# Kernel optimization log

Measured on AMD Instinct MI355X. Metric: run time of the kernel, lower is better.

The kernel has to match this reference:

```python
import jax, jax.numpy as jnp
import numpy as np

B, C, N = 4, 64, 100000   # batch, num_bev_features, points per batch
NY, NX = 496, 432         # BEV grid (nz == 1)
PILLAR = 0.16


def setup_inputs() -> dict:
    key = jax.random.key(0)
    k1, k2, k3, k4 = jax.random.split(key, 4)
    point_feature = jax.random.normal(k1, (B, C, N), dtype=jnp.float32)
    # lidar points: [total, 4] = (batch_idx, x, y, z); each batch has exactly N rows
    bidx = jnp.repeat(jnp.arange(B, dtype=jnp.float32), N)[:, None]
    x = jax.random.uniform(k2, (B * N, 1), minval=0.0, maxval=69.12)
    y = jax.random.uniform(k3, (B * N, 1), minval=-39.68, maxval=39.68)
    z = jax.random.uniform(k4, (B * N, 1), minval=-3.0, maxval=1.0)
    points = jnp.concatenate([bidx, x, y, z], axis=1)
    # voxel_coords only used for batch_size = max(col0)+1
    voxel_coords = jnp.concatenate(
        [bidx.astype(jnp.int32),
         jnp.zeros((B * N, 3), dtype=jnp.int32)], axis=1)
    return {"point_feature": point_feature, "points": points,
            "voxel_coords": voxel_coords}


def _scatter_one(feat, pts_b):
    # feat: [C, N], pts_b: [N, 4]
    x = pts_b[:, 1]
    y = pts_b[:, 2]
    x_idx = jnp.clip(jnp.floor((x - x.min()) / PILLAR), 0, NX - 1).astype(jnp.int32)
    y_idx = jnp.clip(jnp.floor((y - y.min()) / PILLAR), 0, NY - 1).astype(jnp.int32)
    grid = jnp.zeros((C, NY, NX), dtype=feat.dtype)
    return grid.at[:, y_idx, x_idx].set(feat)


def reference(point_feature, points, voxel_coords):
    batch_size = point_feature.shape[0]  # == voxel_coords[:,0].max()+1 by construction
    n = point_feature.shape[2]
    # points are laid out contiguously per batch (col0 == batch idx), so the
    # boolean mask `lidar[:,0]==b` is equivalent to this reshape.
    pts = points.reshape(batch_size, n, points.shape[1])
    spatial_features = jax.vmap(_scatter_one)(point_feature, pts)  # [B, C, NY, NX]
    return spatial_features
```

## Files before the change

kernel.cpp:

```cpp
#include <hip/hip_runtime.h>
#include <stdint.h>

#define BATCH 4
#define CH 64
#define NPT 100000
#define NY 496
#define NX 432
#define NYNX (NY * NX)
#define INV_PILLAR 6.25f

typedef float vfloat4 __attribute__((ext_vector_type(4)));

#define MINBITS_OFF 0
#define WINNER_OFF  256
#define WINNER_BYTES ((size_t)BATCH * NYNX * sizeof(int))
#define FEATT_OFF   ((WINNER_OFF + WINNER_BYTES + 255) & ~(size_t)255)
#define FEATT_BYTES ((size_t)BATCH * (NPT + 1) * CH * sizeof(unsigned short))
#define WS_NEEDED   (FEATT_OFF + FEATT_BYTES)

__device__ __forceinline__ unsigned int f2sortable(float f) {
    unsigned int u = __float_as_uint(f);
    return (u & 0x80000000u) ? ~u : (u | 0x80000000u);
}
__device__ __forceinline__ float sortable2f(unsigned int u) {
    unsigned int b = (u & 0x80000000u) ? (u ^ 0x80000000u) : ~u;
    return __uint_as_float(b);
}
__device__ __forceinline__ unsigned short f2bf(float f) {
    unsigned int u = __float_as_uint(f);
    unsigned int r = u + 0x7FFFu + ((u >> 16) & 1u);
    return (unsigned short)(r >> 16);
}

#define CHUNKS_PER_BATCH 64
#define PTS_PER_CHUNK ((NPT + CHUNKS_PER_BATCH - 1) / CHUNKS_PER_BATCH)

__global__ void minred_kernel(const float* __restrict__ points,
                              unsigned int* __restrict__ minbits) {
    int b = blockIdx.x / CHUNKS_PER_BATCH;
    int chunk = blockIdx.x % CHUNKS_PER_BATCH;
    int lo = chunk * PTS_PER_CHUNK;
    int hi = min(lo + PTS_PER_CHUNK, NPT);
    const vfloat4* pts = (const vfloat4*)points + (size_t)b * NPT;
    float mx = 3.0e38f, my = 3.0e38f;
    for (int i = lo + threadIdx.x; i < hi; i += blockDim.x) {
        vfloat4 p = pts[i];
        mx = fminf(mx, p.y);
        my = fminf(my, p.z);
    }
    #pragma unroll
    for (int off = 32; off; off >>= 1) {
        mx = fminf(mx, __shfl_xor(mx, off));
        my = fminf(my, __shfl_xor(my, off));
    }
    if ((threadIdx.x & 63) == 0) {
        atomicMin(&minbits[2 * b],     f2sortable(mx));
        atomicMin(&minbits[2 * b + 1], f2sortable(my));
    }
}

__global__ void winner_kernel(const float* __restrict__ points,
                              const unsigned int* __restrict__ minbits,
                              int* __restrict__ winner) {
    int i = blockIdx.x * blockDim.x + threadIdx.x;
    if (i >= BATCH * NPT) return;
    int b = i / NPT;
    int li = i - b * NPT;
    vfloat4 p = ((const vfloat4*)points)[i];
    float xmin = sortable2f(minbits[2 * b]);
    float ymin = sortable2f(minbits[2 * b + 1]);
    float fx = fminf(fmaxf(floorf((p.y - xmin) * INV_PILLAR), 0.0f), (float)(NX - 1));
    float fy = fminf(fmaxf(floorf((p.z - ymin) * INV_PILLAR), 0.0f), (float)(NY - 1));
    int xi = (int)fx;
    int yi = (int)fy;
    atomicMax(&winner[(b * NY + yi) * NX + xi], li + 1);
}

#define NTILES ((NPT + 1 + 63) / 64)
__global__ void transpose_kernel(const float* __restrict__ feat,
                                 unsigned short* __restrict__ feat_t) {
    __shared__ float tile[CH][65];
    int b = blockIdx.x / NTILES;
    int n0 = (blockIdx.x % NTILES) * 64;
    int t = threadIdx.x;

    int l16 = t & 15;
    int crow = t >> 4;
    int nt4 = l16 * 4;
    if (n0 + nt4 + 3 < NPT) {
        #pragma unroll
        for (int k = 0; k < 4; ++k) {
            int c = crow + 16 * k;
            vfloat4 v = __builtin_nontemporal_load(
                (const vfloat4*)(feat + ((size_t)b * CH + c) * NPT + n0 + nt4));
            tile[c][nt4 + 0] = v.x;
            tile[c][nt4 + 1] = v.y;
            tile[c][nt4 + 2] = v.z;
            tile[c][nt4 + 3] = v.w;
        }
    } else {
        #pragma unroll
        for (int k = 0; k < 4; ++k) {
            int c = crow + 16 * k;
            for (int j = 0; j < 4; ++j) {
                int n = n0 + nt4 + j;
                tile[c][nt4 + j] = (n < NPT) ? feat[((size_t)b * CH + c) * NPT + n] : 0.0f;
            }
        }
    }
    __syncthreads();

    int c8 = (t & 7) * 8;
    int nr = t >> 3;
    #pragma unroll
    for (int k = 0; k < 2; ++k) {
        int nit = nr + 32 * k;
        int n = n0 + nit;
        if (n < NPT) {
            unsigned int w0 = (unsigned int)f2bf(tile[c8 + 0][nit]) |
                              ((unsigned int)f2bf(tile[c8 + 1][nit]) << 16);
            unsigned int w1 = (unsigned int)f2bf(tile[c8 + 2][nit]) |
                              ((unsigned int)f2bf(tile[c8 + 3][nit]) << 16);
            unsigned int w2 = (unsigned int)f2bf(tile[c8 + 4][nit]) |
                              ((unsigned int)f2bf(tile[c8 + 5][nit]) << 16);
            unsigned int w3 = (unsigned int)f2bf(tile[c8 + 6][nit]) |
                              ((unsigned int)f2bf(tile[c8 + 7][nit]) << 16);
            *(uint4*)(feat_t + ((size_t)b * (NPT + 1) + n) * CH + c8) =
                make_uint4(w0, w1, w2, w3);
        } else if (n == NPT) {
            *(uint4*)(feat_t + ((size_t)b * (NPT + 1) + n) * CH + c8) =
                make_uint4(0u, 0u, 0u, 0u);
        }
    }
}

#define QUADS_PER_BATCH (NYNX / 4)
__global__ void scatter_kernel(const unsigned short* __restrict__ feat_t,
                               const int* __restrict__ winner,
                               float* __restrict__ out) {
    int s = blockIdx.x * blockDim.x + threadIdx.x;
    if (s >= BATCH * QUADS_PER_BATCH) return;
    int b = s / QUADS_PER_BATCH;
    int yx0 = (s - b * QUADS_PER_BATCH) * 4;
    int4 w4 = *(const int4*)(winner + (size_t)b * NYNX + yx0);
    const unsigned short* fb = feat_t + (size_t)b * (NPT + 1) * CH;
    int wv[4] = {w4.x, w4.y, w4.z, w4.w};
    const uint4* col[4];
    #pragma unroll
    for (int i = 0; i < 4; ++i) {
        int c = (wv[i] < 0) ? NPT : (wv[i] - 1);
        col[i] = (const uint4*)(fb + (size_t)c * CH);
    }
    float* ob = out + (size_t)b * CH * NYNX + yx0;
    #pragma unroll
    for (int g = 0; g < 4; ++g) {
        uint4 ua[4], ub[4];
        #pragma unroll
        for (int i = 0; i < 4; ++i) {
            ua[i] = col[i][2 * g];
            ub[i] = col[i][2 * g + 1];
        }
        #pragma unroll
        for (int c = 0; c < 16; ++c) {
            int pair = c >> 1;
            vfloat4 v;
            #pragma unroll
            for (int i = 0; i < 4; ++i) {
                unsigned int src = (pair < 4) ? (&ua[i].x)[pair] : (&ub[i].x)[pair - 4];
                v[i] = __uint_as_float((c & 1) ? (src & 0xFFFF0000u) : (src << 16));
            }
            __builtin_nontemporal_store(
                v, (vfloat4*)(ob + (size_t)(16 * g + c) * NYNX));
        }
    }
}

__global__ void scatter_fallback_kernel(const float* __restrict__ feat,
                                        const int* __restrict__ winner,
                                        float* __restrict__ out) {
    int cell = blockIdx.x * blockDim.x + threadIdx.x;
    if (cell >= BATCH * NYNX) return;
    int b = cell / NYNX;
    int yx = cell - b * NYNX;
    int w = winner[cell];
    int ws_ = (w > 0) ? (w - 1) : 0;
    const float* fb = feat + (size_t)b * CH * NPT;
    float* ob = out + (size_t)b * CH * NYNX + yx;
    #pragma unroll 16
    for (int c = 0; c < CH; ++c) {
        float v = fb[(size_t)c * NPT + ws_];
        ob[(size_t)c * NYNX] = (w > 0) ? v : 0.0f;
    }
}

extern "C" void kernel_launch(void* const* d_in, const int* in_sizes, int n_in,
                              void* d_out, int out_size, void* d_ws, size_t ws_size,
                              hipStream_t stream) {
    const float* point_feature = (const float*)d_in[0];
    const float* points        = (const float*)d_in[1];
    float* out = (float*)d_out;

    unsigned int*   minbits = (unsigned int*)((char*)d_ws + MINBITS_OFF);
    int*            winner  = (int*)((char*)d_ws + WINNER_OFF);
    unsigned short* feat_t  = (unsigned short*)((char*)d_ws + FEATT_OFF);

    (void)hipMemsetAsync(d_ws, 0xFF, WINNER_OFF + WINNER_BYTES, stream);

    minred_kernel<<<BATCH * CHUNKS_PER_BATCH, 256, 0, stream>>>(points, minbits);

    int npts = BATCH * NPT;
    winner_kernel<<<(npts + 255) / 256, 256, 0, stream>>>(points, minbits, winner);

    if (ws_size >= WS_NEEDED) {
        transpose_kernel<<<BATCH * NTILES, 256, 0, stream>>>(point_feature, feat_t);
        int nquad = BATCH * QUADS_PER_BATCH;
        scatter_kernel<<<(nquad + 255) / 256, 256, 0, stream>>>(feat_t, winner, out);
    } else {
        int ncell = BATCH * NYNX;
        scatter_fallback_kernel<<<(ncell + 255) / 256, 256, 0, stream>>>(
            point_feature, winner, out);
    }
}
```

Baseline: 354.9 us.

## Fuse memset, min-reduction and transpose into one prep kernel; drop atomics for mins

Merges the workspace memset, the per-batch min reduction and the feature transpose into a single prep kernel. Per-chunk minimums are written as partials, and every winner block re-reduces them from those partials, which removes the sortable-float atomicMin. The ws_size fallback path is removed. This cuts launch count and one memset pass, at the cost of extra branching in the prep kernel and a redundant partial reduction in each winner block.

After: 329.5 us. 7.2% less time.

```diff
diff --git a/kernel.cpp b/kernel.cpp
--- a/kernel.cpp
+++ b/kernel.cpp
@@ -11,81 +11,73 @@
 
 typedef float vfloat4 __attribute__((ext_vector_type(4)));
 
-#define MINBITS_OFF 0
-#define WINNER_OFF  256
+#define PARTIALS_OFF 0
+#define WINNER_OFF   4096
 #define WINNER_BYTES ((size_t)BATCH * NYNX * sizeof(int))
-#define FEATT_OFF   ((WINNER_OFF + WINNER_BYTES + 255) & ~(size_t)255)
-#define FEATT_BYTES ((size_t)BATCH * (NPT + 1) * CH * sizeof(unsigned short))
-#define WS_NEEDED   (FEATT_OFF + FEATT_BYTES)
-
-__device__ __forceinline__ unsigned int f2sortable(float f) {
-    unsigned int u = __float_as_uint(f);
-    return (u & 0x80000000u) ? ~u : (u | 0x80000000u);
-}
-__device__ __forceinline__ float sortable2f(unsigned int u) {
-    unsigned int b = (u & 0x80000000u) ? (u ^ 0x80000000u) : ~u;
-    return __uint_as_float(b);
-}
+#define FEATT_OFF    ((WINNER_OFF + WINNER_BYTES + 255) & ~(size_t)255)
+#define FEATT_BYTES  ((size_t)BATCH * (NPT + 1) * CH * sizeof(unsigned short))
+#define WS_NEEDED    (FEATT_OFF + FEATT_BYTES)
+
+#define CHUNKS_PER_BATCH 64
+#define PTS_PER_CHUNK ((NPT + CHUNKS_PER_BATCH - 1) / CHUNKS_PER_BATCH)
+#define NTILES ((NPT + 1 + 63) / 64)
+#define K1_GRID (BATCH * NTILES)
+#define QUADS_PER_BATCH (NYNX / 4)
+
 __device__ __forceinline__ unsigned short f2bf(float f) {
     unsigned int u = __float_as_uint(f);
     unsigned int r = u + 0x7FFFu + ((u >> 16) & 1u);
     return (unsigned short)(r >> 16);
 }
 
-#define CHUNKS_PER_BATCH 64
-#define PTS_PER_CHUNK ((NPT + CHUNKS_PER_BATCH - 1) / CHUNKS_PER_BATCH)
-
-__global__ void minred_kernel(const float* __restrict__ points,
-                              unsigned int* __restrict__ minbits) {
-    int b = blockIdx.x / CHUNKS_PER_BATCH;
-    int chunk = blockIdx.x % CHUNKS_PER_BATCH;
-    int lo = chunk * PTS_PER_CHUNK;
-    int hi = min(lo + PTS_PER_CHUNK, NPT);
-    const vfloat4* pts = (const vfloat4*)points + (size_t)b * NPT;
-    float mx = 3.0e38f, my = 3.0e38f;
-    for (int i = lo + threadIdx.x; i < hi; i += blockDim.x) {
-        vfloat4 p = pts[i];
-        mx = fminf(mx, p.y);
-        my = fminf(my, p.z);
-    }
-    #pragma unroll
-    for (int off = 32; off; off >>= 1) {
-        mx = fminf(mx, __shfl_xor(mx, off));
-        my = fminf(my, __shfl_xor(my, off));
-    }
-    if ((threadIdx.x & 63) == 0) {
-        atomicMin(&minbits[2 * b],     f2sortable(mx));
-        atomicMin(&minbits[2 * b + 1], f2sortable(my));
-    }
-}
-
-__global__ void winner_kernel(const float* __restrict__ points,
-                              const unsigned int* __restrict__ minbits,
-                              int* __restrict__ winner) {
-    int i = blockIdx.x * blockDim.x + threadIdx.x;
-    if (i >= BATCH * NPT) return;
-    int b = i / NPT;
-    int li = i - b * NPT;
-    vfloat4 p = ((const vfloat4*)points)[i];
-    float xmin = sortable2f(minbits[2 * b]);
-    float ymin = sortable2f(minbits[2 * b + 1]);
-    float fx = fminf(fmaxf(floorf((p.y - xmin) * INV_PILLAR), 0.0f), (float)(NX - 1));
-    float fy = fminf(fmaxf(floorf((p.z - ymin) * INV_PILLAR), 0.0f), (float)(NY - 1));
-    int xi = (int)fx;
-    int yi = (int)fy;
-    atomicMax(&winner[(b * NY + yi) * NX + xi], li + 1);
-}
-
-#define NTILES ((NPT + 1 + 63) / 64)
-__global__ void transpose_kernel(const float* __restrict__ feat,
-                                 unsigned short* __restrict__ feat_t) {
+__global__ void __launch_bounds__(256)
+prep_kernel(const float* __restrict__ feat,
+            const float* __restrict__ points,
+            float* __restrict__ partials,
+            int* __restrict__ winner,
+            unsigned short* __restrict__ feat_t) {
+    int tid = threadIdx.x;
+    int bid = blockIdx.x;
+
     __shared__ float tile[CH][65];
-    int b = blockIdx.x / NTILES;
-    int n0 = (blockIdx.x % NTILES) * 64;
-    int t = threadIdx.x;
-
-    int l16 = t & 15;
-    int crow = t >> 4;
+    __shared__ float wred[8];
+
+    {
+        int i = bid * 256 + tid;
+        if (i < BATCH * NYNX) winner[i] = -1;
+    }
+
+    if (bid < BATCH * CHUNKS_PER_BATCH) {
+        int b = bid >> 6, chunk = bid & 63;
+        int lo = chunk * PTS_PER_CHUNK;
+        int hi = min(lo + PTS_PER_CHUNK, NPT);
+        const vfloat4* pts = (const vfloat4*)points + (size_t)b * NPT;
+        float mx = 3.0e38f, my = 3.0e38f;
+        for (int i = lo + tid; i < hi; i += 256) {
+            vfloat4 p = pts[i];
+            mx = fminf(mx, p.y);
+            my = fminf(my, p.z);
+        }
+        #pragma unroll
+        for (int off = 32; off; off >>= 1) {
+            mx = fminf(mx, __shfl_xor(mx, off));
+            my = fminf(my, __shfl_xor(my, off));
+        }
+        if ((tid & 63) == 0) { wred[(tid >> 6) * 2] = mx; wred[(tid >> 6) * 2 + 1] = my; }
+        __syncthreads();
+        if (tid == 0) {
+            float ax = fminf(fminf(wred[0], wred[2]), fminf(wred[4], wred[6]));
+            float ay = fminf(fminf(wred[1], wred[3]), fminf(wred[5], wred[7]));
+            partials[(b * CHUNKS_PER_BATCH + chunk) * 2 + 0] = ax;
+            partials[(b * CHUNKS_PER_BATCH + chunk) * 2 + 1] = ay;
+        }
+        __syncthreads();
+    }
+
+    int b = bid / NTILES;
+    int n0 = (bid % NTILES) * 64;
+    int l16 = tid & 15;
+    int crow = tid >> 4;
     int nt4 = l16 * 4;
     if (n0 + nt4 + 3 < NPT) {
         #pragma unroll
@@ -109,9 +101,8 @@
         }
     }
     __syncthreads();
-
-    int c8 = (t & 7) * 8;
-    int nr = t >> 3;
+    int c8 = (tid & 7) * 8;
+    int nr = tid >> 3;
     #pragma unroll
     for (int k = 0; k < 2; ++k) {
         int nit = nr + 32 * k;
@@ -134,10 +125,40 @@
     }
 }
 
-#define QUADS_PER_BATCH (NYNX / 4)
-__global__ void scatter_kernel(const unsigned short* __restrict__ feat_t,
-                               const int* __restrict__ winner,
-                               float* __restrict__ out) {
+__global__ void __launch_bounds__(256)
+winner_kernel(const float* __restrict__ points,
+              const float* __restrict__ partials,
+              int* __restrict__ winner) {
+    __shared__ float bmin[BATCH][2];
+    int tid = threadIdx.x;
+    {
+        int wave = tid >> 6, lane = tid & 63;
+        float px = partials[(wave * CHUNKS_PER_BATCH + lane) * 2 + 0];
+        float py = partials[(wave * CHUNKS_PER_BATCH + lane) * 2 + 1];
+        #pragma unroll
+        for (int off = 32; off; off >>= 1) {
+            px = fminf(px, __shfl_xor(px, off));
+            py = fminf(py, __shfl_xor(py, off));
+        }
+        if (lane == 0) { bmin[wave][0] = px; bmin[wave][1] = py; }
+    }
+    __syncthreads();
+    int i = blockIdx.x * 256 + tid;
+    if (i >= BATCH * NPT) return;
+    int b = i / NPT;
+    int li = i - b * NPT;
+    vfloat4 p = ((const vfloat4*)points)[i];
+    float fx = fminf(fmaxf(floorf((p.y - bmin[b][0]) * INV_PILLAR), 0.0f), (float)(NX - 1));
+    float fy = fminf(fmaxf(floorf((p.z - bmin[b][1]) * INV_PILLAR), 0.0f), (float)(NY - 1));
+    int xi = (int)fx;
+    int yi = (int)fy;
+    atomicMax(&winner[(b * NY + yi) * NX + xi], li + 1);
+}
+
+__global__ void __launch_bounds__(256)
+scatter_kernel(const unsigned short* __restrict__ feat_t,
+               const int* __restrict__ winner,
+               float* __restrict__ out) {
     int s = blockIdx.x * blockDim.x + threadIdx.x;
     if (s >= BATCH * QUADS_PER_BATCH) return;
     int b = s / QUADS_PER_BATCH;
@@ -175,24 +196,6 @@
     }
 }
 
-__global__ void scatter_fallback_kernel(const float* __restrict__ feat,
-                                        const int* __restrict__ winner,
-                                        float* __restrict__ out) {
-    int cell = blockIdx.x * blockDim.x + threadIdx.x;
-    if (cell >= BATCH * NYNX) return;
-    int b = cell / NYNX;
-    int yx = cell - b * NYNX;
-    int w = winner[cell];
-    int ws_ = (w > 0) ? (w - 1) : 0;
-    const float* fb = feat + (size_t)b * CH * NPT;
-    float* ob = out + (size_t)b * CH * NYNX + yx;
-    #pragma unroll 16
-    for (int c = 0; c < CH; ++c) {
-        float v = fb[(size_t)c * NPT + ws_];
-        ob[(size_t)c * NYNX] = (w > 0) ? v : 0.0f;
-    }
-}
-
 extern "C" void kernel_launch(void* const* d_in, const int* in_sizes, int n_in,
                               void* d_out, int out_size, void* d_ws, size_t ws_size,
                               hipStream_t stream) {
@@ -200,24 +203,16 @@
     const float* points        = (const float*)d_in[1];
     float* out = (float*)d_out;
 
-    unsigned int*   minbits = (unsigned int*)((char*)d_ws + MINBITS_OFF);
-    int*            winner  = (int*)((char*)d_ws + WINNER_OFF);
-    unsigned short* feat_t  = (unsigned short*)((char*)d_ws + FEATT_OFF);
-
-    (void)hipMemsetAsync(d_ws, 0xFF, WINNER_OFF + WINNER_BYTES, stream);
-
-    minred_kernel<<<BATCH * CHUNKS_PER_BATCH, 256, 0, stream>>>(points, minbits);
+    float*          partials = (float*)((char*)d_ws + PARTIALS_OFF);
+    int*            winner   = (int*)((char*)d_ws + WINNER_OFF);
+    unsigned short* feat_t   = (unsigned short*)((char*)d_ws + FEATT_OFF);
+
+    prep_kernel<<<K1_GRID, 256, 0, stream>>>(point_feature, points,
+                                             partials, winner, feat_t);
 
     int npts = BATCH * NPT;
-    winner_kernel<<<(npts + 255) / 256, 256, 0, stream>>>(points, minbits, winner);
-
-    if (ws_size >= WS_NEEDED) {
-        transpose_kernel<<<BATCH * NTILES, 256, 0, stream>>>(point_feature, feat_t);
-        int nquad = BATCH * QUADS_PER_BATCH;
-        scatter_kernel<<<(nquad + 255) / 256, 256, 0, stream>>>(feat_t, winner, out);
-    } else {
-        int ncell = BATCH * NYNX;
-        scatter_fallback_kernel<<<(ncell + 255) / 256, 256, 0, stream>>>(
-            point_feature, winner, out);
-    }
-}
+    winner_kernel<<<(npts + 255) / 256, 256, 0, stream>>>(points, partials, winner);
+
+    int nquad = BATCH * QUADS_PER_BATCH;
+    scatter_kernel<<<(nquad + 255) / 256, 256, 0, stream>>>(feat_t, winner, out);
+}
```
